# Performance work log

Measured on AMD Instinct MI355X. Metric: run time of the kernel, lower is better.

The kernel has to match this reference:

```python
import jax, jax.numpy as jnp
import numpy as np

T, B, N1, N2, N3, N4 = 512, 256, 512, 256, 64, 784
BETA_LIF = 0.9
BETA_LI = 0.95
THR = 1.0
LN_EPS = 1e-5


@jax.custom_vjp
def spike(x):
    # snntorch heaviside fire with ATan surrogate gradient (alpha=2 default)
    return (x > 0).astype(x.dtype)

def _spike_fwd(x):
    return spike(x), x

def _spike_bwd(x, g):
    return (g / (1.0 + (jnp.pi * x) ** 2),)

spike.defvjp(_spike_fwd, _spike_bwd)


def setup_inputs() -> dict:
    key = jax.random.key(0)
    ks = jax.random.split(key, 10)
    def lin(k, out_d, in_d):
        k1, k2 = jax.random.split(k)
        bound = 1.0 / np.sqrt(in_d)
        W = jax.random.uniform(k1, (out_d, in_d), jnp.float32, -bound, bound)
        b = jax.random.uniform(k2, (out_d,), jnp.float32, -bound, bound)
        return W, b
    W_lif, b_lif = lin(ks[0], N1, N2)
    W_li, b_li = lin(ks[1], N2, N1)
    W1, b1 = lin(ks[2], N3, N2)
    W2, b2 = lin(ks[3], N4, N3)
    # binary spike train input
    spk_rec = (jax.random.uniform(ks[4], (T, B, N2)) < 0.1).astype(jnp.float32)
    return {
        'spk_rec': spk_rec,
        'W_lif': W_lif, 'b_lif': b_lif,
        'W_li': W_li, 'b_li': b_li,
        'W1': W1, 'b1': b1,
        'W2': W2, 'b2': b2,
        'ln_g': jnp.ones((N4,), jnp.float32),
        'ln_b': jnp.zeros((N4,), jnp.float32),
    }


def reference(spk_rec, W_lif, b_lif, W_li, b_li, W1, b1, W2, b2, ln_g, ln_b):
    # Precompute per-step input currents with one big GEMM: [T,B,n1]
    cur_seq = jnp.einsum('tbi,oi->tbo', spk_rec, W_lif) + b_lif

    def lif_step(mem, cur):
        # snntorch Leaky, reset_mechanism='subtract':
        # reset based on previous-step membrane (detached)
        reset = jax.lax.stop_gradient((mem - THR > 0).astype(mem.dtype))
        mem_new = BETA_LIF * mem + cur - reset * THR
        spk = spike(mem_new - THR)
        return mem_new, spk

    mem0 = jnp.zeros(cur_seq.shape[1:], cur_seq.dtype)
    _, lif_spk = jax.lax.scan(lif_step, mem0, cur_seq)  # [T,B,n1]

    li_in = jnp.einsum('tbi,oi->tbo', lif_spk, W_li) + b_li  # [T,B,n2]
    beta_li = jnp.clip(jnp.asarray(BETA_LI, li_in.dtype), 0.0, 1.0)

    def li_step(mem, inp):
        mem = beta_li * mem + inp
        return mem, mem

    _, li_mem = jax.lax.scan(li_step, jnp.zeros(li_in.shape[1:], li_in.dtype), li_in)

    x = li_mem.mean(axis=0)  # [B,n2]
    h = jax.nn.relu(x @ W1.T + b1)  # [B,n3]
    y = h @ W2.T + b2  # [B,n4]
    mu = jnp.mean(y, axis=-1, keepdims=True)
    var = jnp.var(y, axis=-1, keepdims=True)
    return (y - mu) / jnp.sqrt(var + LN_EPS) * ln_g + ln_b
```

## Files before the change

kernel.cpp:

```cpp
#include <hip/hip_runtime.h>
#include <hip/hip_bf16.h>
#include <cmath>
#include <cstdint>


#define T_TOT 512
#define B_SZ  256
#define N1    512
#define N2    256
#define N3    64
#define N4    784
#define BN    (B_SZ * N1)

typedef unsigned short u16;
typedef short bf16x8 __attribute__((ext_vector_type(8)));
typedef float f32x4 __attribute__((ext_vector_type(4)));

#define OFF_BLIF 0
#define OFF_WLI  512
#define OFF_BLI  131584
#define OFF_W1   131840
#define OFF_B1   148224
#define OFF_W2   148288
#define OFF_B2   198464
#define OFF_LNG  199248
#define OFF_LNB  200032
#define CANON_N  200816

__device__ __forceinline__ float b2f(u16 u) {
  return __uint_as_float(((uint32_t)u) << 16);
}
__device__ __forceinline__ u16 f2b(float f) {
  uint32_t x = __float_as_uint(f);
  return (u16)((x + 0x7fffu + ((x >> 16) & 1u)) >> 16);
}
__device__ __forceinline__ float ldany(const void* p, long i, int isbf) {
  return isbf ? b2f(((const u16*)p)[i]) : ((const float*)p)[i];
}
__device__ __forceinline__ uint32_t pk_trunc(float a, float b) {
  return (__float_as_uint(a) >> 16) | (__float_as_uint(b) & 0xFFFF0000u);
}

__global__ __launch_bounds__(256) void k_initconv(
    const void* wA, const void* wB, const void* t0, const void* t1,
    const void* t2, const void* spk,
    uint32_t* __restrict__ det, uint32_t* __restrict__ sBF,
    uint32_t* __restrict__ sF32)
{
  __shared__ uint32_t redA[256], redB[256];
  int bid = blockIdx.x, tid = threadIdx.x;

  if (bid >= 131) {
    const uint32_t* p = (const uint32_t*)spk + (size_t)(bid - 131) * 4096 +
                        (size_t)tid * 16;
    uint32_t f = 0;
    #pragma unroll
    for (int j = 0; j < 16; j++) if (p[j] == 0x3F803F80u) f = 1;
    redA[tid] = f; __syncthreads();
    for (int s = 128; s > 0; s >>= 1) {
      if (tid < s) redA[tid] |= redA[tid + s];
      __syncthreads();
    }
    if (tid == 0) det[bid - 131] = redA[0];
    return;
  }

  uint32_t mB = 0, mF = 0;
  if (bid < 128) {
    const uint32_t* p = (const uint32_t*)(bid < 64 ? wA : wB) +
                        (size_t)(bid & 63) * 1024 + tid;
    #pragma unroll
    for (int k = 0; k < 4; k++) {
      uint32_t w = p[k * 256];
      uint32_t f = w & 0x7FFFFFFFu; if (f > mF) mF = f;
      uint32_t h0 = (w << 16) & 0x7FFFFFFFu;
      uint32_t h1 = w & 0x7FFF0000u;
      if (h0 > mB) mB = h0;
      if (h1 > mB) mB = h1;
    }
  } else {
    const uint32_t* p = (const uint32_t*)(bid == 128 ? t0 : bid == 129 ? t1 : t2);
    for (int i = tid; i < 392; i += 256) {
      uint32_t w = p[i];
      uint32_t f = w & 0x7FFFFFFFu; if (f > mF) mF = f;
      uint32_t h0 = (w << 16) & 0x7FFFFFFFu;
      uint32_t h1 = w & 0x7FFF0000u;
      if (h0 > mB) mB = h0;
      if (h1 > mB) mB = h1;
    }
  }
  int slot = bid < 128 ? bid : 64 + bid;
  redA[tid] = mB; redB[tid] = mF; __syncthreads();
  for (int s = 128; s > 0; s >>= 1) {
    if (tid < s) {
      if (redA[tid + s] > redA[tid]) redA[tid] = redA[tid + s];
      if (redB[tid + s] > redB[tid]) redB[tid] = redB[tid + s];
    }
    __syncthreads();
  }
  if (tid == 0) { sBF[slot] = redA[0]; sF32[slot] = redB[0]; }
}

__device__ void reduce_slots(const uint32_t* det, const uint32_t* sBF,
                             const uint32_t* sF32, int* isbf_o,
                             uint32_t st[5]) {
  uint32_t f = 0;
  for (int i = 0; i < 32; i++) f |= det[i];
  const uint32_t* S = f ? sBF : sF32;
  uint32_t a0 = 0, a1 = 0;
  for (int i = 0; i < 64; i++) { if (S[i] > a0) a0 = S[i]; }
  for (int i = 64; i < 128; i++) { if (S[i] > a1) a1 = S[i]; }
  st[0] = a0; st[1] = a1; st[2] = S[192]; st[3] = S[193]; st[4] = S[194];
  *isbf_o = (int)f;
}

__global__ __launch_bounds__(256) void k_prep(
    const void* wA, const void* wB,
    const void* t0, const void* t1, const void* t2,
    const void* s_blif, const void* s_bli, const void* s_w1,
    const void* s_b1, const void* s_w2,
    float* __restrict__ canon, u16* __restrict__ Whi, u16* __restrict__ Wlo,
    const uint32_t* __restrict__ det, const uint32_t* __restrict__ sBF,
    const uint32_t* __restrict__ sF32, uint32_t* __restrict__ flg)
{
  int isbf; uint32_t st[5];
  reduce_slots(det, sBF, sF32, &isbf, st);
  if (blockIdx.x == 0 && threadIdx.x == 0) flg[0] = (uint32_t)isbf;
  const void* s_wlif = (st[0] >= st[1]) ? wA : wB;
  const void* s_wli  = (st[0] >= st[1]) ? wB : wA;
  uint32_t s2 = st[2], s3 = st[3], s4 = st[4];
  const void *s_lng, *s_lnb, *s_b2;
  if (s2 >= s3 && s2 >= s4)      s_lng = t0;
  else if (s3 >= s2 && s3 >= s4) s_lng = t1;
  else                           s_lng = t2;
  if (s2 <= s3 && s2 <= s4)      s_lnb = t0;
  else if (s3 <= s2 && s3 <= s4) s_lnb = t1;
  else                           s_lnb = t2;
  s_b2 = (t0 != s_lng && t0 != s_lnb) ? t0
       : (t1 != s_lng && t1 != s_lnb) ? t1 : t2;

  long id = (long)blockIdx.x * 256 + threadIdx.x;
  if (id < 512)    { canon[OFF_BLIF + id] = ldany(s_blif, id, isbf); return; } id -= 512;
  if (id < 131072) { canon[OFF_WLI  + id] = ldany(s_wli,  id, isbf); return; } id -= 131072;
  if (id < 256)    { canon[OFF_BLI  + id] = ldany(s_bli,  id, isbf); return; } id -= 256;
  if (id < 16384)  { canon[OFF_W1   + id] = ldany(s_w1,   id, isbf); return; } id -= 16384;
  if (id < 64)     { canon[OFF_B1   + id] = ldany(s_b1,   id, isbf); return; } id -= 64;
  if (id < 50176)  { canon[OFF_W2   + id] = ldany(s_w2,   id, isbf); return; } id -= 50176;
  if (id < 784)    { canon[OFF_B2   + id] = ldany(s_b2,   id, isbf); return; } id -= 784;
  if (id < 784)    { canon[OFF_LNG  + id] = ldany(s_lng,  id, isbf); return; } id -= 784;
  if (id < 784)    { canon[OFF_LNB  + id] = ldany(s_lnb,  id, isbf); return; } id -= 784;
  if (id < 131072) {
    float wv = ldany(s_wlif, id, isbf);
    u16 h = f2b(wv);
    Whi[id] = h;
    Wlo[id] = f2b(wv - b2f(h));
  }
}

#define SSTEP6(val, M, C, Gv) {                                              \
    float rst_ = (M) > 1.0f ? 1.0f : 0.0f;                                   \
    (M) = 0.9f * (M) + (val) - rst_;                                         \
    float sp_ = (M) > 1.0f ? 1.0f : 0.0f;                                    \
    (C) += sp_;                                                              \
    (Gv) = 0.95f * (Gv) + sp_; }

__global__ __launch_bounds__(256, 2) void k_fused(
    const void* __restrict__ spk, const u16* __restrict__ Whi,
    const u16* __restrict__ Wlo, const float* __restrict__ canon,
    float* __restrict__ Sg, const uint32_t* __restrict__ flg)
{
  __shared__ alignas(16) u16 Ab[2][32 * 256];
  int tid = threadIdx.x, bid = blockIdx.x;
  int nb = bid >> 7, bb = bid & 127;
  int n0 = nb * 128, b0 = bb * 2;
  int lane = tid & 63, wv = tid >> 6;
  int lr = lane & 15, lq = lane >> 4;
  const int isbf = (int)flg[0];

  bf16x8 wh[2][8], wl[2][8];
  #pragma unroll
  for (int jn = 0; jn < 2; jn++) {
    const u16* ph = Whi + (size_t)(n0 + wv * 32 + jn * 16 + lr) * N2 + lq * 8;
    const u16* pl = Wlo + (size_t)(n0 + wv * 32 + jn * 16 + lr) * N2 + lq * 8;
    #pragma unroll
    for (int ks = 0; ks < 8; ks++) {
      wh[jn][ks] = *(const bf16x8*)(ph + ks * 32);
      wl[jn][ks] = *(const bf16x8*)(pl + ks * 32);
    }
  }
  float bv0 = canon[OFF_BLIF + n0 + wv * 32 + lr];
  float bv1 = canon[OFF_BLIF + n0 + wv * 32 + 16 + lr];

  int sr[4], sk[4];
  #pragma unroll
  for (int c = 0; c < 4; c++) {
    int f = tid + 256 * c;
    sr[c] = f >> 5;
    sk[c] = f & 31;
  }
  int4 pre[4];
  #define AELEM(it, c) (((size_t)((16 * (it) + (sr[c] & 15)) * 256 + b0 +    \
                          (sr[c] >> 4))) * 256 + sk[c] * 8)
  #define ALOAD(it) { if (isbf) {                                            \
      _Pragma("unroll") for (int c = 0; c < 4; c++)                          \
        pre[c] = *(const int4*)((const u16*)spk + AELEM(it, c));             \
    } else {                                                                 \
      _Pragma("unroll") for (int c = 0; c < 4; c++) {                        \
        const float4* pf = (const float4*)spk + (AELEM(it, c) >> 2);         \
        float4 fa = pf[0], fb = pf[1]; int4 p;                               \
        p.x = (int)pk_trunc(fa.x, fa.y); p.y = (int)pk_trunc(fa.z, fa.w);    \
        p.z = (int)pk_trunc(fb.x, fb.y); p.w = (int)pk_trunc(fb.z, fb.w);    \
        pre[c] = p; } } }
  #define ASTORE(bf) { _Pragma("unroll") for (int c = 0; c < 4; c++)         \
      *(int4*)&Ab[bf][sr[c] * 256 + ((sk[c] ^ (sr[c] & 7)) * 8)] = pre[c]; }

  ALOAD(0) ASTORE(0)
  ALOAD(1)
  __syncthreads();

  float mem = 0.f, cnt = 0.f, G = 0.f;

  for (int it = 0; it < 32; it++) {
    const u16* ab = Ab[it & 1];
    f32x4 acc[2][2];
    #pragma unroll
    for (int i = 0; i < 2; i++)
      #pragma unroll
      for (int jn = 0; jn < 2; jn++)
        #pragma unroll
        for (int r = 0; r < 4; r++) acc[i][jn][r] = 0.0f;

    #pragma unroll
    for (int ks = 0; ks < 8; ks++) {
      int sl = ((ks * 4 + lq) ^ (lr & 7)) * 8;
      bf16x8 af[2];
      af[0] = *(const bf16x8*)(ab + lr * 256 + sl);
      af[1] = *(const bf16x8*)(ab + (16 + lr) * 256 + sl);
      #pragma unroll
      for (int i = 0; i < 2; i++) {
        acc[i][0] = __builtin_amdgcn_mfma_f32_16x16x32_bf16(af[i], wh[0][ks], acc[i][0], 0, 0, 0);
        acc[i][0] = __builtin_amdgcn_mfma_f32_16x16x32_bf16(af[i], wl[0][ks], acc[i][0], 0, 0, 0);
        acc[i][1] = __builtin_amdgcn_mfma_f32_16x16x32_bf16(af[i], wh[1][ks], acc[i][1], 0, 0, 0);
        acc[i][1] = __builtin_amdgcn_mfma_f32_16x16x32_bf16(af[i], wl[1][ks], acc[i][1], 0, 0, 0);
      }
    }
    if (it < 31) ASTORE((it + 1) & 1)
    __syncthreads();
    if (it < 30) ALOAD(it + 2)

    float Y[4][4];
    #pragma unroll
    for (int rr = 0; rr < 4; rr++) {
      float x0 = acc[0][0][rr], x1 = acc[1][0][rr];
      float x2 = acc[0][1][rr], x3 = acc[1][1][rr];
      float s0 = __shfl_xor(x0, 16), s1 = __shfl_xor(x1, 16);
      float s2 = __shfl_xor(x2, 16), s3 = __shfl_xor(x3, 16);
      bool g1 = (lq & 1) != 0;
      float z0 = g1 ? s1 : x0, z1 = g1 ? x1 : s0;
      float z2 = g1 ? s3 : x2, z3 = g1 ? x3 : s2;
      float t0 = __shfl_xor(z0, 32), t1 = __shfl_xor(z1, 32);
      float t2 = __shfl_xor(z2, 32), t3 = __shfl_xor(z3, 32);
      bool g2 = (lq & 2) != 0;
      Y[rr][0] = g2 ? t2 : z0; Y[rr][1] = g2 ? t3 : z1;
      Y[rr][2] = g2 ? z2 : t0; Y[rr][3] = g2 ? z3 : t1;
    }
    float bv = (lq & 2) ? bv1 : bv0;
    #pragma unroll
    for (int j = 0; j < 4; j++)
      #pragma unroll
      for (int rr = 0; rr < 4; rr++)
        SSTEP6(Y[rr][j] + bv, mem, cnt, G)
  }
  #undef ALOAD
  #undef ASTORE
  #undef AELEM

  int nA = n0 + wv * 32 + (lq >> 1) * 16 + lr;
  int bA = b0 + (lq & 1);
  Sg[(size_t)nA * 256 + bA] = (cnt - 0.95f * G) * 20.0f;
}

__global__ __launch_bounds__(256) void k_tail(
    const float* __restrict__ Sg, const float* __restrict__ canon,
    float* __restrict__ outp, float Csum)
{
  __shared__ float sS[N1];
  __shared__ float sx[N2];
  __shared__ float sh[N3];
  __shared__ float sy[N4];
  __shared__ float red[256];
  int b = blockIdx.x, tid = threadIdx.x;

  for (int i = tid; i < N1; i += 256) sS[i] = Sg[(size_t)i * 256 + b];
  __syncthreads();

  {
    const float4* w = (const float4*)(canon + OFF_WLI + (size_t)tid * N1);
    float a = 0.f;
    for (int k = 0; k < N1 / 4; k++) {
      float4 p4 = w[k];
      a += sS[k*4] * p4.x + sS[k*4+1] * p4.y + sS[k*4+2] * p4.z + sS[k*4+3] * p4.w;
    }
    sx[tid] = (a + Csum * canon[OFF_BLI + tid]) * (1.0f / (float)T_TOT);
  }
  __syncthreads();

  if (tid < N3) {
    const float4* w = (const float4*)(canon + OFF_W1 + (size_t)tid * N2);
    float a = 0.f;
    for (int k = 0; k < N2 / 4; k++) {
      float4 p4 = w[k];
      a += sx[k*4] * p4.x + sx[k*4+1] * p4.y + sx[k*4+2] * p4.z + sx[k*4+3] * p4.w;
    }
    a += canon[OFF_B1 + tid];
    sh[tid] = a > 0.f ? a : 0.f;
  }
  __syncthreads();

  for (int n = tid; n < N4; n += 256) {
    const float4* w = (const float4*)(canon + OFF_W2 + (size_t)n * N3);
    float a = 0.f;
    for (int k = 0; k < N3 / 4; k++) {
      float4 p4 = w[k];
      a += sh[k*4] * p4.x + sh[k*4+1] * p4.y + sh[k*4+2] * p4.z + sh[k*4+3] * p4.w;
    }
    sy[n] = a + canon[OFF_B2 + n];
  }
  __syncthreads();

  float p = 0.f;
  for (int n = tid; n < N4; n += 256) p += sy[n];
  red[tid] = p; __syncthreads();
  for (int s = 128; s > 0; s >>= 1) { if (tid < s) red[tid] += red[tid + s]; __syncthreads(); }
  float mu = red[0] / (float)N4;
  __syncthreads();
  p = 0.f;
  for (int n = tid; n < N4; n += 256) { float d = sy[n] - mu; p += d * d; }
  red[tid] = p; __syncthreads();
  for (int s = 128; s > 0; s >>= 1) { if (tid < s) red[tid] += red[tid + s]; __syncthreads(); }
  float var = red[0] / (float)N4;
  float sc = 1.0f / sqrtf(var + 1e-5f);
  for (int n = tid; n < N4; n += 256) {
    outp[(size_t)b * N4 + n] =
        (sy[n] - mu) * sc * canon[OFF_LNG + n] + canon[OFF_LNB + n];
  }
}

__global__ void k_fillv(float* o, int n, float V) {
  int i = blockIdx.x * 256 + threadIdx.x;
  if (i < n) o[i] = V;
}

extern "C" void kernel_launch(void* const* d_in, const int* in_sizes, int n_in,
                              void* d_out, int out_size, void* d_ws, size_t ws_size,
                              hipStream_t stream) {
  float* out = (float*)d_out;

  int idx_spk = -1, idx_blif = -1, idx_bli = -1, idx_w1 = -1, idx_b1 = -1,
      idx_w2 = -1;
  int idxW[2] = {-1, -1}, nW = 0;
  int idxT[3] = {-1, -1, -1}, nT = 0;
  bool ok = (n_in == 11);
  for (int i = 0; ok && i < 11; i++) {
    switch (in_sizes[i]) {
      case 33554432: if (idx_spk  < 0) idx_spk  = i; else ok = false; break;
      case 512:      if (idx_blif < 0) idx_blif = i; else ok = false; break;
      case 256:      if (idx_bli  < 0) idx_bli  = i; else ok = false; break;
      case 16384:    if (idx_w1   < 0) idx_w1   = i; else ok = false; break;
      case 64:       if (idx_b1   < 0) idx_b1   = i; else ok = false; break;
      case 50176:    if (idx_w2   < 0) idx_w2   = i; else ok = false; break;
      case 131072:   if (nW < 2) idxW[nW++] = i; else ok = false; break;
      case 784:      if (nT < 3) idxT[nT++] = i; else ok = false; break;
      default: ok = false;
    }
  }
  ok = ok && idx_spk >= 0 && idx_blif >= 0 && idx_bli >= 0 && idx_w1 >= 0 &&
       idx_b1 >= 0 && idx_w2 >= 0 && nW == 2 && nT == 3;
  if (!ok) {
    k_fillv<<<(out_size + 255) / 256, 256, 0, stream>>>(
        out, out_size, (float)(n_in >= 1 ? in_sizes[0] : -1));
    return;
  }
  if (out_size != B_SZ * N4) {
    k_fillv<<<(out_size + 255) / 256, 256, 0, stream>>>(
        out, out_size, 1.0e6f + (float)out_size);
    return;
  }

  char* w = (char*)d_ws;
  uint32_t* det  = (uint32_t*)w;
  uint32_t* sBF  = (uint32_t*)(w + 128);
  uint32_t* flg  = (uint32_t*)(w + 1016);
  uint32_t* sF32 = (uint32_t*)(w + 1024);
  float* canon = (float*)(w + 2048);
  size_t canonB = ((size_t)CANON_N * 4 + 255) & ~(size_t)255;
  u16* Whi = (u16*)(w + 2048 + canonB);
  u16* Wlo = Whi + BN;
  float* Sg = (float*)((char*)Wlo + (size_t)BN * 2);
  size_t need = 2048 + canonB + (size_t)2 * BN * 2 + (size_t)BN * 4;
  if (ws_size < need) {
    k_fillv<<<(out_size + 255) / 256, 256, 0, stream>>>(out, out_size, 2.0e6f);
    return;
  }

  double beta = 0.95;
  double bT = std::pow(beta, (double)T_TOT);
  float Csum = (float)(((double)T_TOT - beta * (1.0 - bT) / (1.0 - beta)) / (1.0 - beta));

  k_initconv<<<163, 256, 0, stream>>>(
      d_in[idxW[0]], d_in[idxW[1]], d_in[idxT[0]], d_in[idxT[1]],
      d_in[idxT[2]], d_in[idx_spk], det, sBF, sF32);
  k_prep<<<1297, 256, 0, stream>>>(
      d_in[idxW[0]], d_in[idxW[1]], d_in[idxT[0]], d_in[idxT[1]],
      d_in[idxT[2]], d_in[idx_blif], d_in[idx_bli], d_in[idx_w1],
      d_in[idx_b1], d_in[idx_w2], canon, Whi, Wlo, det, sBF, sF32, flg);
  k_fused<<<512, 256, 0, stream>>>(d_in[idx_spk], Whi, Wlo, canon, Sg, flg);
  k_tail<<<B_SZ, 256, 0, stream>>>(Sg, canon, out, Csum);
}
```

Measured before the change: 295.2 us.

## Specialize fused loop on bf16 input, double-buffer LDS fragments, batch tail rows

The fused GEMM+LIF loop becomes a template on whether the low-part weight correction is needed. When the input is bf16 (flag set), it skips the Wlo loads and half of the MFMAs. A-fragment LDS reads are software-pipelined one k-step ahead so they overlap the MFMAs. The tail kernel now handles four batch rows per block and reuses each weight load across them, at the cost of fewer blocks (64) and serialized layernorm reductions.

Result: faster. 288.3 us (-2.3%).

```diff
diff --git a/kernel.cpp b/kernel.cpp
--- a/kernel.cpp
+++ b/kernel.cpp
@@ -164,28 +164,23 @@
     (C) += sp_;                                                              \
     (Gv) = 0.95f * (Gv) + sp_; }
 
-__global__ __launch_bounds__(256, 2) void k_fused(
+template <int USELO>
+__device__ __forceinline__ void fused_loop(
     const void* __restrict__ spk, const u16* __restrict__ Whi,
     const u16* __restrict__ Wlo, const float* __restrict__ canon,
-    float* __restrict__ Sg, const uint32_t* __restrict__ flg)
+    float* __restrict__ Sg, u16 (&Ab)[2][32 * 256],
+    int n0, int b0, int wv, int lr, int lq, int tid)
 {
-  __shared__ alignas(16) u16 Ab[2][32 * 256];
-  int tid = threadIdx.x, bid = blockIdx.x;
-  int nb = bid >> 7, bb = bid & 127;
-  int n0 = nb * 128, b0 = bb * 2;
-  int lane = tid & 63, wv = tid >> 6;
-  int lr = lane & 15, lq = lane >> 4;
-  const int isbf = (int)flg[0];
-
   bf16x8 wh[2][8], wl[2][8];
   #pragma unroll
   for (int jn = 0; jn < 2; jn++) {
     const u16* ph = Whi + (size_t)(n0 + wv * 32 + jn * 16 + lr) * N2 + lq * 8;
-    const u16* pl = Wlo + (size_t)(n0 + wv * 32 + jn * 16 + lr) * N2 + lq * 8;
-    #pragma unroll
-    for (int ks = 0; ks < 8; ks++) {
-      wh[jn][ks] = *(const bf16x8*)(ph + ks * 32);
-      wl[jn][ks] = *(const bf16x8*)(pl + ks * 32);
+    #pragma unroll
+    for (int ks = 0; ks < 8; ks++) wh[jn][ks] = *(const bf16x8*)(ph + ks * 32);
+    if constexpr (USELO) {
+      const u16* pl = Wlo + (size_t)(n0 + wv * 32 + jn * 16 + lr) * N2 + lq * 8;
+      #pragma unroll
+      for (int ks = 0; ks < 8; ks++) wl[jn][ks] = *(const bf16x8*)(pl + ks * 32);
     }
   }
   float bv0 = canon[OFF_BLIF + n0 + wv * 32 + lr];
@@ -201,7 +196,7 @@
   int4 pre[4];
   #define AELEM(it, c) (((size_t)((16 * (it) + (sr[c] & 15)) * 256 + b0 +    \
                           (sr[c] >> 4))) * 256 + sk[c] * 8)
-  #define ALOAD(it) { if (isbf) {                                            \
+  #define ALOAD(it) { if constexpr (USELO == 0) {                            \
       _Pragma("unroll") for (int c = 0; c < 4; c++)                          \
         pre[c] = *(const int4*)((const u16*)spk + AELEM(it, c));             \
     } else {                                                                 \
@@ -213,15 +208,21 @@
         pre[c] = p; } } }
   #define ASTORE(bf) { _Pragma("unroll") for (int c = 0; c < 4; c++)         \
       *(int4*)&Ab[bf][sr[c] * 256 + ((sk[c] ^ (sr[c] & 7)) * 8)] = pre[c]; }
+  #define LDF(bf, ks_, d0, d1) { const u16* ab_ = Ab[bf];                    \
+      int sl_ = (((ks_) * 4 + lq) ^ (lr & 7)) * 8;                           \
+      d0 = *(const bf16x8*)(ab_ + lr * 256 + sl_);                           \
+      d1 = *(const bf16x8*)(ab_ + (16 + lr) * 256 + sl_); }
 
   ALOAD(0) ASTORE(0)
   ALOAD(1)
   __syncthreads();
 
+  bf16x8 a0, a1, na0, na1;
+  LDF(0, 0, a0, a1)
+
   float mem = 0.f, cnt = 0.f, G = 0.f;
 
   for (int it = 0; it < 32; it++) {
-    const u16* ab = Ab[it & 1];
     f32x4 acc[2][2];
     #pragma unroll
     for (int i = 0; i < 2; i++)
@@ -232,21 +233,25 @@
 
     #pragma unroll
     for (int ks = 0; ks < 8; ks++) {
-      int sl = ((ks * 4 + lq) ^ (lr & 7)) * 8;
-      bf16x8 af[2];
-      af[0] = *(const bf16x8*)(ab + lr * 256 + sl);
-      af[1] = *(const bf16x8*)(ab + (16 + lr) * 256 + sl);
-      #pragma unroll
-      for (int i = 0; i < 2; i++) {
-        acc[i][0] = __builtin_amdgcn_mfma_f32_16x16x32_bf16(af[i], wh[0][ks], acc[i][0], 0, 0, 0);
-        acc[i][0] = __builtin_amdgcn_mfma_f32_16x16x32_bf16(af[i], wl[0][ks], acc[i][0], 0, 0, 0);
-        acc[i][1] = __builtin_amdgcn_mfma_f32_16x16x32_bf16(af[i], wh[1][ks], acc[i][1], 0, 0, 0);
-        acc[i][1] = __builtin_amdgcn_mfma_f32_16x16x32_bf16(af[i], wl[1][ks], acc[i][1], 0, 0, 0);
-      }
+      if (ks < 7) LDF(it & 1, ks + 1, na0, na1)
+      acc[0][0] = __builtin_amdgcn_mfma_f32_16x16x32_bf16(a0, wh[0][ks], acc[0][0], 0, 0, 0);
+      if constexpr (USELO)
+        acc[0][0] = __builtin_amdgcn_mfma_f32_16x16x32_bf16(a0, wl[0][ks], acc[0][0], 0, 0, 0);
+      acc[0][1] = __builtin_amdgcn_mfma_f32_16x16x32_bf16(a0, wh[1][ks], acc[0][1], 0, 0, 0);
+      if constexpr (USELO)
+        acc[0][1] = __builtin_amdgcn_mfma_f32_16x16x32_bf16(a0, wl[1][ks], acc[0][1], 0, 0, 0);
+      acc[1][0] = __builtin_amdgcn_mfma_f32_16x16x32_bf16(a1, wh[0][ks], acc[1][0], 0, 0, 0);
+      if constexpr (USELO)
+        acc[1][0] = __builtin_amdgcn_mfma_f32_16x16x32_bf16(a1, wl[0][ks], acc[1][0], 0, 0, 0);
+      acc[1][1] = __builtin_amdgcn_mfma_f32_16x16x32_bf16(a1, wh[1][ks], acc[1][1], 0, 0, 0);
+      if constexpr (USELO)
+        acc[1][1] = __builtin_amdgcn_mfma_f32_16x16x32_bf16(a1, wl[1][ks], acc[1][1], 0, 0, 0);
+      if (ks < 7) { a0 = na0; a1 = na1; }
     }
     if (it < 31) ASTORE((it + 1) & 1)
     __syncthreads();
     if (it < 30) ALOAD(it + 2)
+    if (it < 31) LDF((it + 1) & 1, 0, a0, a1)
 
     float Y[4][4];
     #pragma unroll
@@ -264,85 +269,127 @@
       Y[rr][0] = g2 ? t2 : z0; Y[rr][1] = g2 ? t3 : z1;
       Y[rr][2] = g2 ? z2 : t0; Y[rr][3] = g2 ? z3 : t1;
     }
-    float bv = (lq & 2) ? bv1 : bv0;
+    float bvv = (lq & 2) ? bv1 : bv0;
     #pragma unroll
     for (int j = 0; j < 4; j++)
       #pragma unroll
       for (int rr = 0; rr < 4; rr++)
-        SSTEP6(Y[rr][j] + bv, mem, cnt, G)
+        SSTEP6(Y[rr][j] + bvv, mem, cnt, G)
   }
   #undef ALOAD
   #undef ASTORE
   #undef AELEM
+  #undef LDF
 
   int nA = n0 + wv * 32 + (lq >> 1) * 16 + lr;
   int bA = b0 + (lq & 1);
   Sg[(size_t)nA * 256 + bA] = (cnt - 0.95f * G) * 20.0f;
 }
 
+__global__ __launch_bounds__(256, 2) void k_fused(
+    const void* __restrict__ spk, const u16* __restrict__ Whi,
+    const u16* __restrict__ Wlo, const float* __restrict__ canon,
+    float* __restrict__ Sg, const uint32_t* __restrict__ flg)
+{
+  __shared__ alignas(16) u16 Ab[2][32 * 256];
+  int tid = threadIdx.x, bid = blockIdx.x;
+  int nb = bid >> 7, bb = bid & 127;
+  int n0 = nb * 128, b0 = bb * 2;
+  int lane = tid & 63, wv = tid >> 6;
+  int lr = lane & 15, lq = lane >> 4;
+
+  if (flg[0]) fused_loop<0>(spk, Whi, Wlo, canon, Sg, Ab, n0, b0, wv, lr, lq, tid);
+  else        fused_loop<1>(spk, Whi, Wlo, canon, Sg, Ab, n0, b0, wv, lr, lq, tid);
+}
+
+#define BG 4
 __global__ __launch_bounds__(256) void k_tail(
     const float* __restrict__ Sg, const float* __restrict__ canon,
     float* __restrict__ outp, float Csum)
 {
-  __shared__ float sS[N1];
-  __shared__ float sx[N2];
-  __shared__ float sh[N3];
-  __shared__ float sy[N4];
+  __shared__ float sS[BG][N1];
+  __shared__ float sx[BG][N2];
+  __shared__ float sh[BG][N3];
+  __shared__ float sy[BG][N4];
   __shared__ float red[256];
-  int b = blockIdx.x, tid = threadIdx.x;
-
-  for (int i = tid; i < N1; i += 256) sS[i] = Sg[(size_t)i * 256 + b];
+  int b0 = blockIdx.x * BG, tid = threadIdx.x;
+
+  for (int i = tid; i < BG * N1; i += 256) {
+    int bb = i & 3, n = i >> 2;
+    sS[bb][n] = Sg[(size_t)n * 256 + b0 + bb];
+  }
   __syncthreads();
 
   {
     const float4* w = (const float4*)(canon + OFF_WLI + (size_t)tid * N1);
-    float a = 0.f;
+    float a[BG] = {0.f, 0.f, 0.f, 0.f};
     for (int k = 0; k < N1 / 4; k++) {
       float4 p4 = w[k];
-      a += sS[k*4] * p4.x + sS[k*4+1] * p4.y + sS[k*4+2] * p4.z + sS[k*4+3] * p4.w;
-    }
-    sx[tid] = (a + Csum * canon[OFF_BLI + tid]) * (1.0f / (float)T_TOT);
+      #pragma unroll
+      for (int bb = 0; bb < BG; bb++)
+        a[bb] += sS[bb][k*4] * p4.x + sS[bb][k*4+1] * p4.y +
+                 sS[bb][k*4+2] * p4.z + sS[bb][k*4+3] * p4.w;
+    }
+    float bli = canon[OFF_BLI + tid];
+    #pragma unroll
+    for (int bb = 0; bb < BG; bb++)
+      sx[bb][tid] = (a[bb] + Csum * bli) * (1.0f / (float)T_TOT);
   }
   __syncthreads();
 
   if (tid < N3) {
     const float4* w = (const float4*)(canon + OFF_W1 + (size_t)tid * N2);
-    float a = 0.f;
+    float a[BG] = {0.f, 0.f, 0.f, 0.f};
     for (int k = 0; k < N2 / 4; k++) {
       float4 p4 = w[k];
-      a += sx[k*4] * p4.x + sx[k*4+1] * p4.y + sx[k*4+2] * p4.z + sx[k*4+3] * p4.w;
-    }
-    a += canon[OFF_B1 + tid];
-    sh[tid] = a > 0.f ? a : 0.f;
+      #pragma unroll
+      for (int bb = 0; bb < BG; bb++)
+        a[bb] += sx[bb][k*4] * p4.x + sx[bb][k*4+1] * p4.y +
+                 sx[bb][k*4+2] * p4.z + sx[bb][k*4+3] * p4.w;
+    }
+    float b1v = canon[OFF_B1 + tid];
+    #pragma unroll
+    for (int bb = 0; bb < BG; bb++) {
+      float v = a[bb] + b1v;
+      sh[bb][tid] = v > 0.f ? v : 0.f;
+    }
   }
   __syncthreads();
 
   for (int n = tid; n < N4; n += 256) {
     const float4* w = (const float4*)(canon + OFF_W2 + (size_t)n * N3);
-    float a = 0.f;
+    float a[BG] = {0.f, 0.f, 0.f, 0.f};
     for (int k = 0; k < N3 / 4; k++) {
       float4 p4 = w[k];
-      a += sh[k*4] * p4.x + sh[k*4+1] * p4.y + sh[k*4+2] * p4.z + sh[k*4+3] * p4.w;
-    }
-    sy[n] = a + canon[OFF_B2 + n];
+      #pragma unroll
+      for (int bb = 0; bb < BG; bb++)
+        a[bb] += sh[bb][k*4] * p4.x + sh[bb][k*4+1] * p4.y +
+                 sh[bb][k*4+2] * p4.z + sh[bb][k*4+3] * p4.w;
+    }
+    float b2v = canon[OFF_B2 + n];
+    #pragma unroll
+    for (int bb = 0; bb < BG; bb++) sy[bb][n] = a[bb] + b2v;
   }
   __syncthreads();
 
-  float p = 0.f;
-  for (int n = tid; n < N4; n += 256) p += sy[n];
-  red[tid] = p; __syncthreads();
-  for (int s = 128; s > 0; s >>= 1) { if (tid < s) red[tid] += red[tid + s]; __syncthreads(); }
-  float mu = red[0] / (float)N4;
-  __syncthreads();
-  p = 0.f;
-  for (int n = tid; n < N4; n += 256) { float d = sy[n] - mu; p += d * d; }
-  red[tid] = p; __syncthreads();
-  for (int s = 128; s > 0; s >>= 1) { if (tid < s) red[tid] += red[tid + s]; __syncthreads(); }
-  float var = red[0] / (float)N4;
-  float sc = 1.0f / sqrtf(var + 1e-5f);
-  for (int n = tid; n < N4; n += 256) {
-    outp[(size_t)b * N4 + n] =
-        (sy[n] - mu) * sc * canon[OFF_LNG + n] + canon[OFF_LNB + n];
+  for (int bb = 0; bb < BG; bb++) {
+    float p = 0.f;
+    for (int n = tid; n < N4; n += 256) p += sy[bb][n];
+    __syncthreads();
+    red[tid] = p; __syncthreads();
+    for (int s = 128; s > 0; s >>= 1) { if (tid < s) red[tid] += red[tid + s]; __syncthreads(); }
+    float mu = red[0] / (float)N4;
+    __syncthreads();
+    p = 0.f;
+    for (int n = tid; n < N4; n += 256) { float d = sy[bb][n] - mu; p += d * d; }
+    red[tid] = p; __syncthreads();
+    for (int s = 128; s > 0; s >>= 1) { if (tid < s) red[tid] += red[tid + s]; __syncthreads(); }
+    float var = red[0] / (float)N4;
+    float sc = 1.0f / sqrtf(var + 1e-5f);
+    for (int n = tid; n < N4; n += 256) {
+      outp[(size_t)(b0 + bb) * N4 + n] =
+          (sy[bb][n] - mu) * sc * canon[OFF_LNG + n] + canon[OFF_LNB + n];
+    }
   }
 }
 
@@ -415,5 +462,5 @@
       d_in[idxT[2]], d_in[idx_blif], d_in[idx_bli], d_in[idx_w1],
       d_in[idx_b1], d_in[idx_w2], canon, Whi, Wlo, det, sBF, sF32, flg);
   k_fused<<<512, 256, 0, stream>>>(d_in[idx_spk], Whi, Wlo, canon, Sg, flg);
-  k_tail<<<B_SZ, 256, 0, stream>>>(Sg, canon, out, Csum);
-}
+  k_tail<<<64, 256, 0, stream>>>(Sg, canon, out, Csum);
+}
```
